# Kernel tuning notes

Hardware: AMD Instinct MI355X
Metric: run time of the kernel (lower is better)

## Reference

```python
import jax, jax.numpy as jnp
import numpy as np

EPS = 1e-5
DN = ('NCHW', 'OIHW', 'NCHW')

def _conv(x, w):
    return jax.lax.conv_general_dilated(x, w, (1, 1), 'VALID', dimension_numbers=DN)

def _bn4(x, g, b, m, v):
    # BatchNorm2d in eval mode, per-channel over NCHW
    inv = g / jnp.sqrt(v + EPS)
    return x * inv[None, :, None, None] + (b - m * inv)[None, :, None, None]

def _bn1(x, g, b, m, v):
    inv = g / jnp.sqrt(v + EPS)
    return x * inv[None, :] + (b - m * inv)[None, :]

def _hardtanh(x):
    return jnp.clip(x, -1.0, 1.0)

def _sign(x):
    return jnp.sign(x)

def _maxpool2(x):
    return jax.lax.reduce_window(x, -jnp.inf, jax.lax.max,
                                 (1, 1, 2, 2), (1, 1, 2, 2), 'VALID')

def setup_inputs() -> dict:
    key = jax.random.key(0)
    ks = jax.random.split(key, 20)
    B = 8192
    d = {
        'x': jax.random.normal(ks[0], (B, 8, 16, 16), jnp.float32),
        'w0': jax.random.normal(ks[1], (32, 8, 3, 3), jnp.float32) * 0.1,
        'b0': jax.random.normal(ks[2], (32,), jnp.float32) * 0.1,
        'g1': jax.random.uniform(ks[3], (32,), jnp.float32, 0.5, 1.5),
        'be1': jax.random.normal(ks[4], (32,), jnp.float32) * 0.1,
        'm1': jax.random.normal(ks[5], (32,), jnp.float32) * 0.1,
        'v1': jax.random.uniform(ks[6], (32,), jnp.float32, 0.5, 1.5),
        'w2': jax.random.normal(ks[7], (32, 32, 3, 3), jnp.float32) * 0.1,
        'g2': jax.random.uniform(ks[8], (32,), jnp.float32, 0.5, 1.5),
        'be2': jax.random.normal(ks[9], (32,), jnp.float32) * 0.1,
        'm2': jax.random.normal(ks[10], (32,), jnp.float32) * 0.1,
        'v2': jax.random.uniform(ks[11], (32,), jnp.float32, 0.5, 1.5),
        'w_fc': jax.random.normal(ks[12], (516, 1152), jnp.float32) * 0.03,
        'g3': jax.random.uniform(ks[13], (516,), jnp.float32, 0.5, 1.5),
        'be3': jax.random.normal(ks[14], (516,), jnp.float32) * 0.1,
        'm3': jax.random.normal(ks[15], (516,), jnp.float32) * 0.1,
        'v3': jax.random.uniform(ks[16], (516,), jnp.float32, 0.5, 1.5),
        'w_last': jax.random.normal(ks[17], (10, 516), jnp.float32) * 0.05,
        'b_last': jax.random.normal(ks[18], (10,), jnp.float32) * 0.05,
    }
    return d

def reference(x, w0, b0, g1, be1, m1, v1, w2, g2, be2, m2, v2,
              w_fc, g3, be3, m3, v3, w_last, b_last):
    # initial float conv + BN + Hardtanh
    h = _conv(x, w0) + b0[None, :, None, None]          # [B,32,14,14]
    h = _hardtanh(_bn4(h, g1, be1, m1, v1))
    # binarized conv (sign(input), sign(weight), no bias)
    h = _conv(_sign(h), _sign(w2))                      # [B,32,12,12]
    h = _hardtanh(_bn4(h, g2, be2, m2, v2))
    h = _maxpool2(h)                                    # [B,32,6,6]
    # dropout is identity in eval mode
    h = h.reshape(h.shape[0], -1)                       # [B,1152]
    # binarized linear (no bias)
    h = _sign(h) @ _sign(w_fc).T                        # [B,516]
    h = _hardtanh(_bn1(h, g3, be3, m3, v3))
    return h @ w_last.T + b_last[None, :]               # [B,10]
```

## Files before the change

kernel.cpp:

```cpp
#include <hip/hip_runtime.h>
#include <cstdint>

#define EPSF 1e-5f

typedef __attribute__((ext_vector_type(8))) short short8;
typedef __attribute__((ext_vector_type(4))) float f32x4;
typedef __attribute__((ext_vector_type(4))) unsigned int u32x4;

__device__ inline uint32_t bf16rne(float x) {
    uint32_t u = __builtin_bit_cast(uint32_t, x);
    return (u + 0x7fffu + ((u >> 16) & 1u)) >> 16;
}
__device__ inline float bf16f(uint32_t b) {
    return __builtin_bit_cast(float, b << 16);
}

__device__ __noinline__ bool recheck_sign(const float* __restrict__ xim,
                                          const float* __restrict__ w0,
                                          int py, int px, int co,
                                          float ivc, float offc)
{
    double ad = 0.0;
    for (int ci = 0; ci < 8; ci++)
        for (int ky = 0; ky < 3; ky++)
            for (int kx = 0; kx < 3; kx++)
                ad = fma((double)xim[ci * 256 + (py + ky) * 16 + px + kx],
                         (double)w0[co * 72 + ci * 9 + ky * 3 + kx], ad);
    return (ad * (double)ivc + (double)offc) < 0.0;
}

__global__ __launch_bounds__(256, 4) void convAP(
    const float* __restrict__ x, const float* __restrict__ w0,
    const float* __restrict__ b0, const float* __restrict__ g1,
    const float* __restrict__ be1, const float* __restrict__ m1,
    const float* __restrict__ v1,
    const float* __restrict__ w2, const float* __restrict__ wfc,
    const float* __restrict__ g3, const float* __restrict__ be3,
    const float* __restrict__ m3, const float* __restrict__ v3,
    const float* __restrict__ wlast,
    uint32_t* __restrict__ s1bits, uint32_t* __restrict__ w2bits,
    uint32_t* __restrict__ wfcb, float* __restrict__ inv3p,
    float* __restrict__ sh3p, float* __restrict__ wlt)
{
    __shared__ __align__(16) char lds[4][9216];
    const int t = threadIdx.x;

    if (blockIdx.x >= 1024) {
        int pb = blockIdx.x - 1024;
        if (pb < 129) {
            const int wid = t >> 6, lane2 = t & 63;
            const int j = pb * 4 + wid;
            const int c = lane2 & 31, pp = lane2 >> 5;
            const float* row = wfc + j * 1152 + c * 36;
            #pragma unroll
            for (int i = 0; i < 18; i++) {
                int pos = 2 * i + pp;
                float v = row[pos];
                unsigned long long mb = __ballot(v < 0.f);
                if (lane2 == 0)  wfcb[(2 * i) * 576 + j]     = (uint32_t)mb;
                if (lane2 == 32) wfcb[(2 * i + 1) * 576 + j] = (uint32_t)(mb >> 32);
            }
            return;
        }
        int id = (pb - 129) * 256 + t;
        if (id < 288) {
            int co = id / 9, r = id % 9;
            uint32_t b = 0;
            for (int ci = 0; ci < 32; ci++)
                b |= (uint32_t)(w2[(co * 32 + ci) * 9 + r] < 0.f) << ci;
            w2bits[id] = b;
            return;
        }
        id -= 288;
        if (id < 576) {
            float iv = 0.f, sh = 0.f;
            if (id < 516) {
                iv = g3[id] / sqrtf(__fadd_rn(v3[id], EPSF));
                sh = __fsub_rn(be3[id], __fmul_rn(m3[id], iv));
            }
            inv3p[id] = iv; sh3p[id] = sh;
            return;
        }
        id -= 576;
        if (id < 5760) {
            int k = id / 576, j = id % 576;
            wlt[id] = (j < 516) ? wlast[k * 516 + j] : 0.f;
            return;
        }
        id -= 5760;
        if (id < 2160) {
            int p = id / 60, j = 516 + id % 60;
            wfcb[p * 576 + j] = 0u;
        }
        return;
    }

    const int wv = t >> 6, lane = t & 63;
    const int g = lane >> 4, n = lane & 15;

    uint32_t* bfl = (uint32_t*)&lds[0][0];
    float2*   bnl = (float2*)(&lds[0][0] + 12288);

    for (int e = t; e < 768; e += 256) {
        int L = e / 12, r = e % 12;
        int nt = r / 6, s = (r % 6) / 2, h = r & 1;
        int gg = L >> 4, nn = L & 15;
        int tap = 4 * s + gg;
        uint32_t d[4] = {0, 0, 0, 0};
        if (tap < 9) {
            int co = nt * 16 + nn;
            #pragma unroll
            for (int j2 = 0; j2 < 4; j2++) {
                float wa = w0[co * 72 + (2 * j2) * 9 + tap];
                float wb = w0[co * 72 + (2 * j2 + 1) * 9 + tap];
                uint32_t ha = bf16rne(wa), hb = bf16rne(wb);
                uint32_t va, vb;
                if (h == 0) { va = ha; vb = hb; }
                else { va = bf16rne(wa - bf16f(ha)); vb = bf16rne(wb - bf16f(hb)); }
                d[j2] = va | (vb << 16);
            }
        }
        *(u32x4*)(bfl + e * 4) = (u32x4){d[0], d[1], d[2], d[3]};
    }
    if (t < 32) {
        float iv = g1[t] / sqrtf(__fadd_rn(v1[t], EPSF));
        float sh = __fsub_rn(be1[t], __fmul_rn(m1[t], iv));
        bnl[t] = make_float2(iv, __fadd_rn(__fmul_rn(b0[t], iv), sh));
    }
    __syncthreads();

    short8 Bh[2][3], Bl[2][3];
    {
        const uint32_t* bb = bfl + lane * 48;
        #pragma unroll
        for (int nt = 0; nt < 2; nt++)
            #pragma unroll
            for (int s = 0; s < 3; s++) {
                Bh[nt][s] = *(const short8*)(bb + (nt * 6 + s * 2) * 4);
                Bl[nt][s] = *(const short8*)(bb + (nt * 6 + s * 2 + 1) * 4);
            }
    }
    const float2 bnA = bnl[n], bnB = bnl[16 + n];
    __syncthreads();

    char* hib = lds[wv];
    char* lob = lds[wv] + 4608;

    if (lane < 32) {
        *(u32x4*)(hib + (256 + lane) * 16) = (u32x4){0, 0, 0, 0};
        *(u32x4*)(lob + (256 + lane) * 16) = (u32x4){0, 0, 0, 0};
    }

    int koff[3];
    #pragma unroll
    for (int s = 0; s < 3; s++) {
        int tap = 4 * s + g;
        koff[s] = (tap < 9) ? ((tap / 3) * 16 + (tap % 3)) * 16 : 0;
    }

    const int imgbase = blockIdx.x * 8 + wv * 2;

    f32x4 pf[8];
    {
        const float* xb = x + (size_t)imgbase * 2048 + lane * 4;
        #pragma unroll
        for (int ci = 0; ci < 8; ci++) pf[ci] = *(const f32x4*)(xb + ci * 256);
    }

    for (int it = 0; it < 2; it++) {
        const int img = imgbase + it;
        const float* xim = x + (size_t)img * 2048;

        #pragma unroll
        for (int e = 0; e < 4; e++) {
            int p = 4 * lane + e;
            uint32_t hw[4], lw[4];
            #pragma unroll
            for (int j2 = 0; j2 < 4; j2++) {
                float a  = pf[2 * j2][e];
                float bv = pf[2 * j2 + 1][e];
                uint32_t ha = bf16rne(a), hb = bf16rne(bv);
                uint32_t la = bf16rne(a - bf16f(ha)), lb = bf16rne(bv - bf16f(hb));
                hw[j2] = ha | (hb << 16);
                lw[j2] = la | (lb << 16);
            }
            *(u32x4*)(hib + p * 16) = (u32x4){hw[0], hw[1], hw[2], hw[3]};
            *(u32x4*)(lob + p * 16) = (u32x4){lw[0], lw[1], lw[2], lw[3]};
        }

        if (it == 0) {
            const float* xb1 = x + (size_t)(imgbase + 1) * 2048 + lane * 4;
            #pragma unroll
            for (int ci = 0; ci < 8; ci++) pf[ci] = *(const f32x4*)(xb1 + ci * 256);
        }

        uint32_t* outb = s1bits + (size_t)img * 196;
        for (int tile = 0; tile < 13; ++tile) {
            int posA = tile * 16 + n;
            int pyA = posA / 14, pxA = posA - pyA * 14;
            int sl = (pyA * 16 + pxA) * 16;

            f32x4 acc0 = {0.f, 0.f, 0.f, 0.f}, acc1 = {0.f, 0.f, 0.f, 0.f};
            #pragma unroll
            for (int s = 0; s < 3; s++) {
                short8 Ah = *(const short8*)(hib + sl + koff[s]);
                short8 Al = *(const short8*)(lob + sl + koff[s]);
                acc0 = __builtin_amdgcn_mfma_f32_16x16x32_bf16(Al, Bh[0][s], acc0, 0, 0, 0);
                acc0 = __builtin_amdgcn_mfma_f32_16x16x32_bf16(Ah, Bl[0][s], acc0, 0, 0, 0);
                acc0 = __builtin_amdgcn_mfma_f32_16x16x32_bf16(Ah, Bh[0][s], acc0, 0, 0, 0);
                acc1 = __builtin_amdgcn_mfma_f32_16x16x32_bf16(Al, Bh[1][s], acc1, 0, 0, 0);
                acc1 = __builtin_amdgcn_mfma_f32_16x16x32_bf16(Ah, Bl[1][s], acc1, 0, 0, 0);
                acc1 = __builtin_amdgcn_mfma_f32_16x16x32_bf16(Ah, Bh[1][s], acc1, 0, 0, 0);
            }

            #pragma unroll
            for (int r = 0; r < 4; r++) {
                int pos = tile * 16 + 4 * g + r;
                float yv0 = fmaf(acc0[r], bnA.x, bnA.y);
                float yv1 = fmaf(acc1[r], bnB.x, bnB.y);
                bool bit0, bit1;
                if (__builtin_expect(pos < 196 && fabsf(yv0) < 3e-4f, 0)) {
                    int py = pos / 14, px = pos - py * 14;
                    bit0 = recheck_sign(xim, w0, py, px, n, bnA.x, bnA.y);
                } else bit0 = (yv0 < 0.f);
                if (__builtin_expect(pos < 196 && fabsf(yv1) < 3e-4f, 0)) {
                    int py = pos / 14, px = pos - py * 14;
                    bit1 = recheck_sign(xim, w0, py, px, 16 + n, bnB.x, bnB.y);
                } else bit1 = (yv1 < 0.f);
                unsigned long long m0 = __ballot(bit0);
                unsigned long long m1 = __ballot(bit1);
                uint32_t word = (uint32_t)((m0 >> (16 * g)) & 0xffffull)
                              | ((uint32_t)((m1 >> (16 * g)) & 0xffffull) << 16);
                if (n == 0 && pos < 196) outb[pos] = word;
            }
        }
    }
}

__global__ __launch_bounds__(256) void convBF(
    const uint32_t* __restrict__ s1bits, const uint32_t* __restrict__ w2bits,
    const float* __restrict__ g2, const float* __restrict__ be2,
    const float* __restrict__ m2, const float* __restrict__ v2,
    const uint32_t* __restrict__ wfcb,
    const float* __restrict__ inv3p, const float* __restrict__ sh3p,
    const float* __restrict__ wlt, const float* __restrict__ blast,
    float* __restrict__ out)
{
    __shared__ uint32_t s1l[8][196];
    __shared__ uint32_t l_in[288];
    const int t = threadIdx.x, wid = t >> 6, lane = t & 63;

    for (int i = t; i < 1568; i += 256)
        ((uint32_t*)s1l)[i] = s1bits[blockIdx.x * 1568 + i];

    const int c = lane & 31, h = lane >> 5;
    uint32_t wr[9];
    #pragma unroll
    for (int k = 0; k < 9; k++) wr[k] = w2bits[c * 9 + k];
    float ivv = g2[c] / sqrtf(__fadd_rn(v2[c], EPSF));
    float shv = __fsub_rn(be2[c], __fmul_rn(m2[c], ivv));
    __syncthreads();

    for (int rep = 0; rep < 2; rep++) {
        const int iml = wid * 2 + rep;
        const uint32_t* s1w = s1l[iml];
        uint32_t* outp = &l_in[iml * 36];

        for (int yy = 0; yy < 3; yy++) {
            const int y2 = yy + 3 * h;
            const int rbase = 2 * y2 * 14;
            uint32_t win[4][4];
            #pragma unroll
            for (int rr = 0; rr < 4; rr++) {
                uint2 a = *(const uint2*)&s1w[rbase + rr * 14];
                uint2 b = *(const uint2*)&s1w[rbase + rr * 14 + 2];
                win[rr][0] = a.x; win[rr][1] = a.y; win[rr][2] = b.x; win[rr][3] = b.y;
            }
            for (int x2 = 0; x2 < 6; x2++) {
                if (x2 > 0) {
                    #pragma unroll
                    for (int rr = 0; rr < 4; rr++) {
                        win[rr][0] = win[rr][2]; win[rr][1] = win[rr][3];
                        uint2 b = *(const uint2*)&s1w[rbase + rr * 14 + 2 * x2 + 2];
                        win[rr][2] = b.x; win[rr][3] = b.y;
                    }
                }
                int mx = -10000;
                #pragma unroll
                for (int dy = 0; dy < 2; dy++)
                    #pragma unroll
                    for (int dx = 0; dx < 2; dx++) {
                        int p = 0;
                        #pragma unroll
                        for (int ky = 0; ky < 3; ky++)
                            #pragma unroll
                            for (int kx = 0; kx < 3; kx++)
                                p += __popc(win[dy + ky][dx + kx] ^ wr[ky * 3 + kx]);
                        mx = max(mx, 288 - 2 * p);
                    }
                float yv = __fadd_rn(__fmul_rn((float)mx, ivv), shv);
                unsigned long long mb = __ballot(yv < 0.f);
                int pos = y2 * 6 + x2;
                if (lane == 0)  outp[pos] = (uint32_t)mb;
                if (lane == 32) outp[pos] = (uint32_t)(mb >> 32);
            }
        }
    }
    __syncthreads();

    const int b0i = blockIdx.x * 8 + wid * 2;
    const uint32_t* in0 = &l_in[wid * 72];

    int pc0[9], pc1[9];
    #pragma unroll
    for (int q = 0; q < 9; q++) { pc0[q] = 0; pc1[q] = 0; }

    for (int w = 0; w < 36; w++) {
        uint32_t i0 = in0[w], i1 = in0[36 + w];
        const uint32_t* wf = wfcb + w * 576 + lane;
        #pragma unroll
        for (int q = 0; q < 9; q++) {
            uint32_t f = wf[q * 64];
            pc0[q] += __popc(i0 ^ f);
            pc1[q] += __popc(i1 ^ f);
        }
    }

    float oa[2][10];
    #pragma unroll
    for (int b = 0; b < 2; b++)
        #pragma unroll
        for (int k = 0; k < 10; k++) oa[b][k] = 0.f;

    #pragma unroll
    for (int q = 0; q < 9; q++) {
        int j = lane + 64 * q;
        float iv3 = inv3p[j], sh3 = sh3p[j];
        float t0 = fminf(1.f, fmaxf(-1.f, __fadd_rn(__fmul_rn((float)(1152 - 2 * pc0[q]), iv3), sh3)));
        float t1 = fminf(1.f, fmaxf(-1.f, __fadd_rn(__fmul_rn((float)(1152 - 2 * pc1[q]), iv3), sh3)));
        #pragma unroll
        for (int k = 0; k < 10; k++) {
            float wvv = wlt[k * 576 + j];
            oa[0][k] = fmaf(t0, wvv, oa[0][k]);
            oa[1][k] = fmaf(t1, wvv, oa[1][k]);
        }
    }

    #pragma unroll
    for (int m = 1; m < 64; m <<= 1)
        #pragma unroll
        for (int b = 0; b < 2; b++)
            #pragma unroll
            for (int k = 0; k < 10; k++)
                oa[b][k] += __shfl_xor(oa[b][k], m, 64);

    if (lane == 0) {
        for (int b = 0; b < 2; b++)
            for (int k = 0; k < 10; k++)
                out[(b0i + b) * 10 + k] = oa[b][k] + blast[k];
    }
}

extern "C" void kernel_launch(void* const* d_in, const int* in_sizes, int n_in,
                              void* d_out, int out_size, void* d_ws, size_t ws_size,
                              hipStream_t stream)
{
    (void)in_sizes; (void)n_in; (void)out_size; (void)ws_size;
    const float* x     = (const float*)d_in[0];
    const float* w0    = (const float*)d_in[1];
    const float* b0    = (const float*)d_in[2];
    const float* g1    = (const float*)d_in[3];
    const float* be1   = (const float*)d_in[4];
    const float* m1    = (const float*)d_in[5];
    const float* v1    = (const float*)d_in[6];
    const float* w2    = (const float*)d_in[7];
    const float* g2    = (const float*)d_in[8];
    const float* be2   = (const float*)d_in[9];
    const float* m2    = (const float*)d_in[10];
    const float* v2    = (const float*)d_in[11];
    const float* wfc   = (const float*)d_in[12];
    const float* g3    = (const float*)d_in[13];
    const float* be3   = (const float*)d_in[14];
    const float* m3    = (const float*)d_in[15];
    const float* v3    = (const float*)d_in[16];
    const float* wlast = (const float*)d_in[17];
    const float* blast = (const float*)d_in[18];

    char* ws = (char*)d_ws;
    uint32_t* s1bits = (uint32_t*)(ws);
    uint32_t* w2bits = (uint32_t*)(ws + 6422528);
    uint32_t* wfcb   = (uint32_t*)(ws + 6423680);
    float*    inv3p  = (float*)(ws + 6506624);
    float*    sh3p   = (float*)(ws + 6508928);
    float*    wlt    = (float*)(ws + 6511232);

    convAP<<<1188, 256, 0, stream>>>(x, w0, b0, g1, be1, m1, v1,
                                     w2, wfc, g3, be3, m3, v3, wlast,
                                     s1bits, w2bits, wfcb, inv3p, sh3p, wlt);
    convBF<<<1024, 256, 0, stream>>>(s1bits, w2bits, g2, be2, m2, v2,
                                     wfcb, inv3p, sh3p, wlt, blast, (float*)d_out);
}
```

Before: 240.7 us.

## Fuse first conv with binarized conv/FC stages and split weight prep kernel

Merges the float conv stage and the binarized conv+FC stage into one kernel. The first-layer sign bits stay in shared memory instead of round-tripping through a global s1bits buffer. Weight preprocessing moves into a separate small kernel that runs before it. Blocks shrink to 128 threads handling 4 images, and the register prefetch of the next image is dropped, so load latency may be less hidden.

```diff
diff --git a/kernel.cpp b/kernel.cpp
--- a/kernel.cpp
+++ b/kernel.cpp
@@ -13,6 +13,62 @@
 }
 __device__ inline float bf16f(uint32_t b) {
     return __builtin_bit_cast(float, b << 16);
+}
+
+__global__ __launch_bounds__(256) void prep_kernel(
+    const float* __restrict__ w2, const float* __restrict__ wfc,
+    const float* __restrict__ g3, const float* __restrict__ be3,
+    const float* __restrict__ m3, const float* __restrict__ v3,
+    const float* __restrict__ wlast,
+    uint32_t* __restrict__ w2bits, uint32_t* __restrict__ wfcb,
+    float* __restrict__ inv3p, float* __restrict__ sh3p, float* __restrict__ wlt)
+{
+    const int tid = threadIdx.x;
+    if (blockIdx.x < 129) {
+        const int wid = tid >> 6, lane2 = tid & 63;
+        const int j = blockIdx.x * 4 + wid;
+        const int c = lane2 & 31, pp = lane2 >> 5;
+        const float* row = wfc + j * 1152 + c * 36;
+        #pragma unroll
+        for (int i = 0; i < 18; i++) {
+            int pos = 2 * i + pp;
+            float v = row[pos];
+            unsigned long long mb = __ballot(v < 0.f);
+            if (lane2 == 0)  wfcb[(2 * i) * 576 + j]     = (uint32_t)mb;
+            if (lane2 == 32) wfcb[(2 * i + 1) * 576 + j] = (uint32_t)(mb >> 32);
+        }
+        return;
+    }
+    int id = (blockIdx.x - 129) * 256 + tid;
+    if (id < 288) {
+        int co = id / 9, r = id % 9;
+        uint32_t b = 0;
+        for (int ci = 0; ci < 32; ci++)
+            b |= (uint32_t)(w2[(co * 32 + ci) * 9 + r] < 0.f) << ci;
+        w2bits[id] = b;
+        return;
+    }
+    id -= 288;
+    if (id < 576) {
+        float iv = 0.f, sh = 0.f;
+        if (id < 516) {
+            iv = g3[id] / sqrtf(__fadd_rn(v3[id], EPSF));
+            sh = __fsub_rn(be3[id], __fmul_rn(m3[id], iv));
+        }
+        inv3p[id] = iv; sh3p[id] = sh;
+        return;
+    }
+    id -= 576;
+    if (id < 5760) {
+        int k = id / 576, j = id % 576;
+        wlt[id] = (j < 516) ? wlast[k * 516 + j] : 0.f;
+        return;
+    }
+    id -= 5760;
+    if (id < 2160) {
+        int p = id / 60, j = 516 + id % 60;
+        wfcb[p * 576 + j] = 0u;
+    }
 }
 
 __device__ __noinline__ bool recheck_sign(const float* __restrict__ xim,
@@ -29,79 +85,31 @@
     return (ad * (double)ivc + (double)offc) < 0.0;
 }
 
-__global__ __launch_bounds__(256, 4) void convAP(
+__global__ __launch_bounds__(128) void fused(
     const float* __restrict__ x, const float* __restrict__ w0,
     const float* __restrict__ b0, const float* __restrict__ g1,
     const float* __restrict__ be1, const float* __restrict__ m1,
     const float* __restrict__ v1,
-    const float* __restrict__ w2, const float* __restrict__ wfc,
-    const float* __restrict__ g3, const float* __restrict__ be3,
-    const float* __restrict__ m3, const float* __restrict__ v3,
-    const float* __restrict__ wlast,
-    uint32_t* __restrict__ s1bits, uint32_t* __restrict__ w2bits,
-    uint32_t* __restrict__ wfcb, float* __restrict__ inv3p,
-    float* __restrict__ sh3p, float* __restrict__ wlt)
+    const uint32_t* __restrict__ w2bits,
+    const float* __restrict__ g2, const float* __restrict__ be2,
+    const float* __restrict__ m2, const float* __restrict__ v2,
+    const uint32_t* __restrict__ wfcb,
+    const float* __restrict__ inv3p, const float* __restrict__ sh3p,
+    const float* __restrict__ wlt, const float* __restrict__ blast,
+    float* __restrict__ out)
 {
-    __shared__ __align__(16) char lds[4][9216];
+    __shared__ __align__(16) char planes[2][9216];
+    __shared__ uint32_t s1l[4][196];
+    __shared__ uint32_t l_in[144];
+
     const int t = threadIdx.x;
-
-    if (blockIdx.x >= 1024) {
-        int pb = blockIdx.x - 1024;
-        if (pb < 129) {
-            const int wid = t >> 6, lane2 = t & 63;
-            const int j = pb * 4 + wid;
-            const int c = lane2 & 31, pp = lane2 >> 5;
-            const float* row = wfc + j * 1152 + c * 36;
-            #pragma unroll
-            for (int i = 0; i < 18; i++) {
-                int pos = 2 * i + pp;
-                float v = row[pos];
-                unsigned long long mb = __ballot(v < 0.f);
-                if (lane2 == 0)  wfcb[(2 * i) * 576 + j]     = (uint32_t)mb;
-                if (lane2 == 32) wfcb[(2 * i + 1) * 576 + j] = (uint32_t)(mb >> 32);
-            }
-            return;
-        }
-        int id = (pb - 129) * 256 + t;
-        if (id < 288) {
-            int co = id / 9, r = id % 9;
-            uint32_t b = 0;
-            for (int ci = 0; ci < 32; ci++)
-                b |= (uint32_t)(w2[(co * 32 + ci) * 9 + r] < 0.f) << ci;
-            w2bits[id] = b;
-            return;
-        }
-        id -= 288;
-        if (id < 576) {
-            float iv = 0.f, sh = 0.f;
-            if (id < 516) {
-                iv = g3[id] / sqrtf(__fadd_rn(v3[id], EPSF));
-                sh = __fsub_rn(be3[id], __fmul_rn(m3[id], iv));
-            }
-            inv3p[id] = iv; sh3p[id] = sh;
-            return;
-        }
-        id -= 576;
-        if (id < 5760) {
-            int k = id / 576, j = id % 576;
-            wlt[id] = (j < 516) ? wlast[k * 516 + j] : 0.f;
-            return;
-        }
-        id -= 5760;
-        if (id < 2160) {
-            int p = id / 60, j = 516 + id % 60;
-            wfcb[p * 576 + j] = 0u;
-        }
-        return;
-    }
-
     const int wv = t >> 6, lane = t & 63;
     const int g = lane >> 4, n = lane & 15;
 
-    uint32_t* bfl = (uint32_t*)&lds[0][0];
-    float2*   bnl = (float2*)(&lds[0][0] + 12288);
-
-    for (int e = t; e < 768; e += 256) {
+    uint32_t* bfl = (uint32_t*)&planes[0][0];
+    float2*   bnl = (float2*)(&planes[0][0] + 12288);
+
+    for (int e = t; e < 768; e += 128) {
         int L = e / 12, r = e % 12;
         int nt = r / 6, s = (r % 6) / 2, h = r & 1;
         int gg = L >> 4, nn = L & 15;
@@ -143,8 +151,8 @@
     const float2 bnA = bnl[n], bnB = bnl[16 + n];
     __syncthreads();
 
-    char* hib = lds[wv];
-    char* lob = lds[wv] + 4608;
+    char* hib = planes[wv];
+    char* lob = planes[wv] + 4608;
 
     if (lane < 32) {
         *(u32x4*)(hib + (256 + lane) * 16) = (u32x4){0, 0, 0, 0};
@@ -158,43 +166,36 @@
         koff[s] = (tap < 9) ? ((tap / 3) * 16 + (tap % 3)) * 16 : 0;
     }
 
-    const int imgbase = blockIdx.x * 8 + wv * 2;
-
-    f32x4 pf[8];
-    {
-        const float* xb = x + (size_t)imgbase * 2048 + lane * 4;
-        #pragma unroll
-        for (int ci = 0; ci < 8; ci++) pf[ci] = *(const f32x4*)(xb + ci * 256);
-    }
+    const int imgbase = blockIdx.x * 4 + wv * 2;
 
     for (int it = 0; it < 2; it++) {
         const int img = imgbase + it;
         const float* xim = x + (size_t)img * 2048;
 
-        #pragma unroll
-        for (int e = 0; e < 4; e++) {
-            int p = 4 * lane + e;
-            uint32_t hw[4], lw[4];
-            #pragma unroll
-            for (int j2 = 0; j2 < 4; j2++) {
-                float a  = pf[2 * j2][e];
-                float bv = pf[2 * j2 + 1][e];
-                uint32_t ha = bf16rne(a), hb = bf16rne(bv);
-                uint32_t la = bf16rne(a - bf16f(ha)), lb = bf16rne(bv - bf16f(hb));
-                hw[j2] = ha | (hb << 16);
-                lw[j2] = la | (lb << 16);
-            }
-            *(u32x4*)(hib + p * 16) = (u32x4){hw[0], hw[1], hw[2], hw[3]};
-            *(u32x4*)(lob + p * 16) = (u32x4){lw[0], lw[1], lw[2], lw[3]};
-        }
-
-        if (it == 0) {
-            const float* xb1 = x + (size_t)(imgbase + 1) * 2048 + lane * 4;
-            #pragma unroll
-            for (int ci = 0; ci < 8; ci++) pf[ci] = *(const f32x4*)(xb1 + ci * 256);
-        }
-
-        uint32_t* outb = s1bits + (size_t)img * 196;
+        {
+            f32x4 pf[8];
+            const float* xb = xim + lane * 4;
+            #pragma unroll
+            for (int ci = 0; ci < 8; ci++) pf[ci] = *(const f32x4*)(xb + ci * 256);
+            #pragma unroll
+            for (int e = 0; e < 4; e++) {
+                int p = 4 * lane + e;
+                uint32_t hw[4], lw[4];
+                #pragma unroll
+                for (int j2 = 0; j2 < 4; j2++) {
+                    float a  = pf[2 * j2][e];
+                    float bv = pf[2 * j2 + 1][e];
+                    uint32_t ha = bf16rne(a), hb = bf16rne(bv);
+                    uint32_t la = bf16rne(a - bf16f(ha)), lb = bf16rne(bv - bf16f(hb));
+                    hw[j2] = ha | (hb << 16);
+                    lw[j2] = la | (lb << 16);
+                }
+                *(u32x4*)(hib + p * 16) = (u32x4){hw[0], hw[1], hw[2], hw[3]};
+                *(u32x4*)(lob + p * 16) = (u32x4){lw[0], lw[1], lw[2], lw[3]};
+            }
+        }
+
+        uint32_t* outb = s1l[wv * 2 + it];
         for (int tile = 0; tile < 13; ++tile) {
             int posA = tile * 16 + n;
             int pyA = posA / 14, pxA = posA - pyA * 14;
@@ -235,23 +236,7 @@
             }
         }
     }
-}
-
-__global__ __launch_bounds__(256) void convBF(
-    const uint32_t* __restrict__ s1bits, const uint32_t* __restrict__ w2bits,
-    const float* __restrict__ g2, const float* __restrict__ be2,
-    const float* __restrict__ m2, const float* __restrict__ v2,
-    const uint32_t* __restrict__ wfcb,
-    const float* __restrict__ inv3p, const float* __restrict__ sh3p,
-    const float* __restrict__ wlt, const float* __restrict__ blast,
-    float* __restrict__ out)
-{
-    __shared__ uint32_t s1l[8][196];
-    __shared__ uint32_t l_in[288];
-    const int t = threadIdx.x, wid = t >> 6, lane = t & 63;
-
-    for (int i = t; i < 1568; i += 256)
-        ((uint32_t*)s1l)[i] = s1bits[blockIdx.x * 1568 + i];
+    __syncthreads();
 
     const int c = lane & 31, h = lane >> 5;
     uint32_t wr[9];
@@ -259,10 +244,9 @@
     for (int k = 0; k < 9; k++) wr[k] = w2bits[c * 9 + k];
     float ivv = g2[c] / sqrtf(__fadd_rn(v2[c], EPSF));
     float shv = __fsub_rn(be2[c], __fmul_rn(m2[c], ivv));
-    __syncthreads();
 
     for (int rep = 0; rep < 2; rep++) {
-        const int iml = wid * 2 + rep;
+        const int iml = wv * 2 + rep;
         const uint32_t* s1w = s1l[iml];
         uint32_t* outp = &l_in[iml * 36];
 
@@ -308,8 +292,8 @@
     }
     __syncthreads();
 
-    const int b0i = blockIdx.x * 8 + wid * 2;
-    const uint32_t* in0 = &l_in[wid * 72];
+    const int b0i = blockIdx.x * 4 + wv * 2;
+    const uint32_t* in0 = &l_in[wv * 72];
 
     int pc0[9], pc1[9];
     #pragma unroll
@@ -387,16 +371,15 @@
     const float* blast = (const float*)d_in[18];
 
     char* ws = (char*)d_ws;
-    uint32_t* s1bits = (uint32_t*)(ws);
-    uint32_t* w2bits = (uint32_t*)(ws + 6422528);
-    uint32_t* wfcb   = (uint32_t*)(ws + 6423680);
-    float*    inv3p  = (float*)(ws + 6506624);
-    float*    sh3p   = (float*)(ws + 6508928);
-    float*    wlt    = (float*)(ws + 6511232);
-
-    convAP<<<1188, 256, 0, stream>>>(x, w0, b0, g1, be1, m1, v1,
-                                     w2, wfc, g3, be3, m3, v3, wlast,
-                                     s1bits, w2bits, wfcb, inv3p, sh3p, wlt);
-    convBF<<<1024, 256, 0, stream>>>(s1bits, w2bits, g2, be2, m2, v2,
-                                     wfcb, inv3p, sh3p, wlt, blast, (float*)d_out);
-}
+    uint32_t* w2bits = (uint32_t*)(ws);
+    uint32_t* wfcb   = (uint32_t*)(ws + 1152);
+    float*    inv3p  = (float*)(ws + 84096);
+    float*    sh3p   = (float*)(ws + 86400);
+    float*    wlt    = (float*)(ws + 88704);
+
+    prep_kernel<<<167, 256, 0, stream>>>(w2, wfc, g3, be3, m3, v3, wlast,
+                                         w2bits, wfcb, inv3p, sh3p, wlt);
+    fused<<<2048, 128, 0, stream>>>(x, w0, b0, g1, be1, m1, v1,
+                                    w2bits, g2, be2, m2, v2,
+                                    wfcb, inv3p, sh3p, wlt, blast, (float*)d_out);
+}
```

New measurement: 254.0 us. 1.06x slower.
